# Performance work log

Measured on AMD Instinct MI355X. Metric: run time of the kernel, lower is better.

Reference implementation:

```python
import jax, jax.numpy as jnp
import numpy as np

N, E = 100000, 1600000
IN_C, OUT_C, H, EDGE_DIM = 128, 64, 2, 4
NEG_SLOPE = 0.2
LN_EPS = 1e-5


def setup_inputs() -> dict:
    key = jax.random.key(0)
    ks = jax.random.split(key, 12)
    s = 1.0 / np.sqrt(IN_C)
    inp = {
        "x": jax.random.normal(ks[0], (N, IN_C), jnp.float32),
        "edge_index": jax.random.randint(ks[1], (2, E), 0, N, jnp.int64),
        "edge_attr": jax.random.normal(ks[2], (E, EDGE_DIM), jnp.float32),
        "W": jax.random.normal(ks[3], (IN_C, H * OUT_C), jnp.float32) * s,
        "att_src": jax.random.normal(ks[4], (H, OUT_C), jnp.float32) * s,
        "att_dst": jax.random.normal(ks[5], (H, OUT_C), jnp.float32) * s,
        "W_edge": jax.random.normal(ks[6], (EDGE_DIM, H * OUT_C), jnp.float32) * 0.5,
        "att_edge": jax.random.normal(ks[7], (H, OUT_C), jnp.float32) * s,
        "bias": jnp.zeros((OUT_C,), jnp.float32),
        "gamma": jnp.ones((OUT_C,), jnp.float32),
        "beta": jnp.zeros((OUT_C,), jnp.float32),
    }
    return inp


def reference(x, edge_index, edge_attr, W, att_src, att_dst, W_edge, att_edge, bias, gamma, beta):
    n = x.shape[0]
    src, dst = edge_index[0], edge_index[1]
    # shared src/dst linear (PyG GATConv with single input tensor)
    h = (x @ W).reshape(n, H, OUT_C)                       # [N,H,C]
    a_src = jnp.einsum("nhc,hc->nh", h, att_src)          # [N,H]
    a_dst = jnp.einsum("nhc,hc->nh", h, att_dst)          # [N,H]
    e = (edge_attr @ W_edge).reshape(-1, H, OUT_C)         # [E,H,C]
    a_edge = jnp.einsum("ehc,hc->eh", e, att_edge)        # [E,H]
    alpha = jax.nn.leaky_relu(a_src[src] + a_dst[dst] + a_edge, NEG_SLOPE)  # [E,H]
    # segment softmax over edges grouped by destination node
    amax = jax.ops.segment_max(alpha, dst, num_segments=n)
    ex = jnp.exp(alpha - amax[dst])
    denom = jax.ops.segment_sum(ex, dst, num_segments=n)
    w = ex / (denom[dst] + 1e-16)                          # [E,H]
    msg = h[src] * w[:, :, None]                           # [E,H,C]
    out = jax.ops.segment_sum(msg, dst, num_segments=n)    # [N,H,C]
    out = out.mean(axis=1) + bias                          # concat=False -> head mean
    # LayerNorm + ReLU
    mu = out.mean(-1, keepdims=True)
    var = ((out - mu) ** 2).mean(-1, keepdims=True)
    out = (out - mu) * jax.lax.rsqrt(var + LN_EPS) * gamma + beta
    return jax.nn.relu(out)
```

## Files before the change

### kernel.cpp

```cpp
#include <hip/hip_runtime.h>
#include <hip/hip_fp16.h>
#include <math.h>

#define IN_C 128
#define HC   128
#define OUT_C 64
#define NEG_SLOPE 0.2f
#define LN_EPS 1e-5f
#define CHUNK 4096
#define BSH   8
#define BMSK  255
#define NBMAX 512
#define NB2MAX 1024

typedef __attribute__((ext_vector_type(8))) short bf16x8;
typedef __attribute__((ext_vector_type(4))) float f32x4;

__device__ inline unsigned bf16pack(float a, float b) {
    unsigned ua = __float_as_uint(a), ub = __float_as_uint(b);
    ua = (ua + 0x7fffu + ((ua >> 16) & 1u)) >> 16;
    ub = (ub + 0x7fffu + ((ub >> 16) & 1u)) >> 16;
    return ua | (ub << 16);
}

__global__ __launch_bounds__(256) void k_pre(const float* __restrict__ W,
                                             const float* __restrict__ W_edge,
                                             const float* __restrict__ att_edge,
                                             const int* __restrict__ ei_dst,
                                             unsigned short* __restrict__ WbfT,
                                             float* __restrict__ V,
                                             int* __restrict__ off,
                                             int E, int NB, int PB) {
    __shared__ int hist[NBMAX];
    int b = blockIdx.x, t = threadIdx.x;
    if (b < 8) {
        #pragma unroll
        for (int i = 0; i < 8; ++i) {
            int idx = b * 2048 + i * 256 + t;
            int k = idx >> 7, col = idx & 127;
            unsigned u = __float_as_uint(W[idx]);
            WbfT[col * 128 + k] =
                (unsigned short)((u + 0x7fffu + ((u >> 16) & 1u)) >> 16);
        }
        return;
    }
    if (b == 8) {
        if (t < 8) {
            int d = t >> 1, h = t & 1;
            float s = 0.f;
            for (int c = 0; c < 64; ++c)
                s += W_edge[d * HC + h * 64 + c] * att_edge[h * 64 + c];
            V[d * 2 + h] = s;
        }
        return;
    }
    int pb = b - 9;
    for (int i = t; i < NB; i += 256) hist[i] = 0;
    __syncthreads();
    int base = pb * CHUNK;
    int lim = E - base; if (lim > CHUNK) lim = CHUNK;
    if (lim == CHUNK) {
        #pragma unroll
        for (int u = 0; u < 4; ++u) {
            int4 v = *(const int4*)&ei_dst[base + u * 1024 + t * 4];
            atomicAdd(&hist[v.x >> BSH], 1);
            atomicAdd(&hist[v.y >> BSH], 1);
            atomicAdd(&hist[v.z >> BSH], 1);
            atomicAdd(&hist[v.w >> BSH], 1);
        }
    } else {
        for (int i = t; i < lim; i += 256)
            atomicAdd(&hist[ei_dst[base + i] >> BSH], 1);
    }
    __syncthreads();
    for (int i = t; i < NB; i += 256)
        off[(size_t)i * PB + pb] = hist[i];
}

__global__ __launch_bounds__(256) void k_scan(int* __restrict__ off,
                                              int* __restrict__ bsum, int nS) {
    __shared__ int sm[256];
    int t = threadIdx.x;
    int base = blockIdx.x * 1024 + t * 4;
    int v0 = 0, v1 = 0, v2 = 0, v3 = 0;
    if (base + 0 < nS) v0 = off[base + 0];
    if (base + 1 < nS) v1 = off[base + 1];
    if (base + 2 < nS) v2 = off[base + 2];
    if (base + 3 < nS) v3 = off[base + 3];
    int s = v0 + v1 + v2 + v3;
    sm[t] = s;
    __syncthreads();
    for (int o = 1; o < 256; o <<= 1) {
        int u = (t >= o) ? sm[t - o] : 0;
        __syncthreads();
        sm[t] += u;
        __syncthreads();
    }
    int excl = sm[t] - s;
    if (base + 0 < nS) off[base + 0] = excl;
    if (base + 1 < nS) off[base + 1] = excl + v0;
    if (base + 2 < nS) off[base + 2] = excl + v0 + v1;
    if (base + 3 < nS) off[base + 3] = excl + v0 + v1 + v2;
    if (t == 255) bsum[blockIdx.x] = sm[255];
}

__device__ inline void scan_bsum(const int* __restrict__ bsum, int nb2,
                                 int* bs, int* sm, int t) {
    int v0 = (4 * t + 0 < nb2) ? bsum[4 * t + 0] : 0;
    int v1 = (4 * t + 1 < nb2) ? bsum[4 * t + 1] : 0;
    int v2 = (4 * t + 2 < nb2) ? bsum[4 * t + 2] : 0;
    int v3 = (4 * t + 3 < nb2) ? bsum[4 * t + 3] : 0;
    int s = v0 + v1 + v2 + v3;
    sm[t] = s;
    __syncthreads();
    for (int o = 1; o < 256; o <<= 1) {
        int u = (t >= o) ? sm[t - o] : 0;
        __syncthreads();
        sm[t] += u;
        __syncthreads();
    }
    int excl = sm[t] - s;
    bs[4 * t + 0] = excl;
    bs[4 * t + 1] = excl + v0;
    bs[4 * t + 2] = excl + v0 + v1;
    bs[4 * t + 3] = excl + v0 + v1 + v2;
    __syncthreads();
}

__global__ __launch_bounds__(256) void k_fused(
        const float* __restrict__ x,
        const unsigned short* __restrict__ WbfT,
        const float* __restrict__ attS, const float* __restrict__ attD,
        unsigned* __restrict__ hb,
        float* __restrict__ a_src, float* __restrict__ a_dst, int M,
        const int* __restrict__ ei, const float* __restrict__ ea,
        const float* __restrict__ V,
        const int* __restrict__ off, const int* __restrict__ bsum,
        int* __restrict__ bsum2, uint2* __restrict__ pA,
        int E, int NB, int PB, int nb2, int GB) {
    __shared__ unsigned xb[64 * 64];
    const int t = threadIdx.x;
    const int bid = blockIdx.x;
    const int r5 = bid % 5, g5 = bid / 5;

    if (r5 == 4) {
        int* cur = (int*)xb;
        int* bs  = (int*)xb + NBMAX;
        int* sm  = (int*)xb + NBMAX + NB2MAX;
        int pb = g5;
        scan_bsum(bsum, nb2, bs, sm, t);
        if (pb == 0)
            for (int i = t; i < nb2; i += 256) bsum2[i] = bs[i];
        for (int i = t; i < NB; i += 256) {
            size_t oi = (size_t)i * PB + pb;
            cur[i] = off[oi] + bs[(int)(oi >> 10)];
        }
        __syncthreads();
        float v0 = V[0], v1 = V[1], v2 = V[2], v3 = V[3];
        float v4 = V[4], v5 = V[5], v6 = V[6], v7 = V[7];
        int base = pb * CHUNK;
        int lim = E - base; if (lim > CHUNK) lim = CHUNK;
        if (lim == CHUNK) {
            #pragma unroll
            for (int h = 0; h < 2; ++h) {
                int e0 = base + h * 2048 + t;
                int sA[8], dA[8];
                #pragma unroll
                for (int k = 0; k < 8; ++k) {
                    sA[k] = ei[e0 + k * 256];
                    dA[k] = ei[E + e0 + k * 256];
                }
                float4 aA[8];
                #pragma unroll
                for (int k = 0; k < 8; ++k)
                    aA[k] = ((const float4*)ea)[e0 + k * 256];
                #pragma unroll
                for (int k = 0; k < 8; ++k) {
                    float ae0 = aA[k].x * v0 + aA[k].y * v2 + aA[k].z * v4 + aA[k].w * v6;
                    float ae1 = aA[k].x * v1 + aA[k].y * v3 + aA[k].z * v5 + aA[k].w * v7;
                    __half2 hx = __floats2half2_rn(ae0, ae1);
                    int slot = atomicAdd(&cur[dA[k] >> BSH], 1);
                    pA[slot] = make_uint2(
                        (unsigned)sA[k] | ((unsigned)(dA[k] & BMSK) << 17),
                        *reinterpret_cast<unsigned*>(&hx));
                }
            }
        } else {
            for (int i = t; i < lim; i += 256) {
                int e = base + i;
                int s = ei[e], d = ei[E + e];
                float4 a = ((const float4*)ea)[e];
                float ae0 = a.x * v0 + a.y * v2 + a.z * v4 + a.w * v6;
                float ae1 = a.x * v1 + a.y * v3 + a.z * v5 + a.w * v7;
                __half2 hx = __floats2half2_rn(ae0, ae1);
                int slot = atomicAdd(&cur[d >> BSH], 1);
                pA[slot] = make_uint2((unsigned)s | ((unsigned)(d & BMSK) << 17),
                                      *reinterpret_cast<unsigned*>(&hx));
            }
        }
        return;
    }

    const int gid = g5 * 4 + r5;
    if (gid >= GB) return;
    const int brow = gid * 64;
    const float4* x4 = (const float4*)x;
    #pragma unroll
    for (int i = 0; i < 8; ++i) {
        int idx = i * 256 + t;
        int row = idx >> 5, c4 = idx & 31;
        float4 v = make_float4(0.f, 0.f, 0.f, 0.f);
        if (brow + row < M) v = x4[(size_t)(brow + row) * 32 + c4];
        unsigned lo = bf16pack(v.x, v.y), hi = bf16pack(v.z, v.w);
        int byte = row * 256 + ((c4 * 8) ^ ((row & 7) << 4));
        *(uint2*)((char*)xb + byte) = make_uint2(lo, hi);
    }
    __syncthreads();

    const int w = t >> 6, lane = t & 63;
    const int col = lane & 15, qr = lane >> 4;
    f32x4 acc[8];
    #pragma unroll
    for (int ct = 0; ct < 8; ++ct) acc[ct] = (f32x4){0.f, 0.f, 0.f, 0.f};

    const int arow = w * 16 + col;
    #pragma unroll
    for (int ks = 0; ks < 4; ++ks) {
        int abyte = arow * 256 + ((ks * 64 + qr * 16) ^ ((arow & 7) << 4));
        bf16x8 af = *(const bf16x8*)((const char*)xb + abyte);
        #pragma unroll
        for (int ct = 0; ct < 8; ++ct) {
            bf16x8 bfr = *(const bf16x8*)&WbfT[(size_t)(ct * 16 + col) * 128 + ks * 32 + qr * 8];
            acc[ct] = __builtin_amdgcn_mfma_f32_16x16x32_bf16(af, bfr, acc[ct], 0, 0, 0);
        }
    }

    float pS0[4], pS1[4], pD0[4], pD1[4];
    #pragma unroll
    for (int r = 0; r < 4; ++r) { pS0[r] = pS1[r] = pD0[r] = pD1[r] = 0.f; }
    #pragma unroll
    for (int ct = 0; ct < 8; ++ct) {
        float s = attS[ct * 16 + col], d = attD[ct * 16 + col];
        #pragma unroll
        for (int r = 0; r < 4; ++r) {
            float a = acc[ct][r];
            if (ct < 4) { pS0[r] += a * s; pD0[r] += a * d; }
            else        { pS1[r] += a * s; pD1[r] += a * d; }
        }
    }
    #pragma unroll
    for (int m = 1; m < 16; m <<= 1) {
        #pragma unroll
        for (int r = 0; r < 4; ++r) {
            pS0[r] += __shfl_xor(pS0[r], m);
            pS1[r] += __shfl_xor(pS1[r], m);
            pD0[r] += __shfl_xor(pD0[r], m);
            pD1[r] += __shfl_xor(pD1[r], m);
        }
    }
    #pragma unroll
    for (int r = 0; r < 4; ++r) {
        int grow = brow + w * 16 + qr * 4 + r;
        if (grow < M) {
            if (col == 0) {
                a_src[2 * grow + 0] = pS0[r];
                a_src[2 * grow + 1] = pS1[r];
                a_dst[2 * grow + 0] = pD0[r];
                a_dst[2 * grow + 1] = pD1[r];
            }
            #pragma unroll
            for (int ct = 0; ct < 4; ++ct)
                hb[(size_t)grow * 64 + ct * 16 + col] =
                    bf16pack(acc[ct][r], acc[ct + 4][r]);
        }
    }
}

__global__ __launch_bounds__(256) void k_csr(const uint2* __restrict__ pA,
                                             const int* __restrict__ off,
                                             const int* __restrict__ bsum2,
                                             const float* __restrict__ a_src,
                                             const float* __restrict__ a_dst,
                                             int* __restrict__ rowptr,
                                             uint2* __restrict__ payload,
                                             int M, int E, int NB, int PB) {
    __shared__ int cnt[256];
    __shared__ int sc[256];
    __shared__ int cur[256];
    __shared__ float2 adl[256];
    int b = blockIdx.x, t = threadIdx.x;
    int n0 = b << BSH;
    int nloc = M - n0; if (nloc > 256) nloc = 256;

    size_t o0 = (size_t)b * PB;
    int s0 = off[o0] + bsum2[(int)(o0 >> 10)];
    int s1 = E;
    if (b + 1 < NB) {
        size_t o1 = (size_t)(b + 1) * PB;
        s1 = off[o1] + bsum2[(int)(o1 >> 10)];
    }
    cnt[t] = 0;
    if (t < nloc) adl[t] = ((const float2*)a_dst)[n0 + t];
    __syncthreads();

    for (int i = s0 + t; i < s1; i += 256)
        atomicAdd(&cnt[(pA[i].x >> 17) & BMSK], 1);
    __syncthreads();
    int c = cnt[t];
    sc[t] = c;
    __syncthreads();
    for (int o = 1; o < 256; o <<= 1) {
        int u = (t >= o) ? sc[t - o] : 0;
        __syncthreads();
        sc[t] += u;
        __syncthreads();
    }
    {
        int base = s0 + sc[t] - c;
        cur[t] = base;
        if (t < nloc) rowptr[n0 + t] = base;
    }
    if (b == NB - 1 && t == 0) rowptr[M] = E;
    __syncthreads();
    for (int i = s0 + t; i < s1; i += 256) {
        uint2 p = pA[i];
        int src = p.x & 0x1FFFF;
        int dl = (p.x >> 17) & BMSK;
        __half2 aeh = *reinterpret_cast<__half2*>(&p.y);
        float2 as = ((const float2*)a_src)[src];
        float2 ad = adl[dl];
        float al0 = as.x + ad.x + __low2float(aeh);
        al0 = al0 > 0.f ? al0 : NEG_SLOPE * al0;
        float al1 = as.y + ad.y + __high2float(aeh);
        al1 = al1 > 0.f ? al1 : NEG_SLOPE * al1;
        __half2 hx = __floats2half2_rn(__expf(al0), __expf(al1));
        int pos = atomicAdd(&cur[dl], 1);
        payload[pos] = make_uint2((unsigned)src, *reinterpret_cast<unsigned*>(&hx));
    }
}

__global__ __launch_bounds__(256) void k_gather(const uint2* __restrict__ payload,
                                                const int* __restrict__ rowptr,
                                                const unsigned* __restrict__ hb,
                                                const float* __restrict__ bias,
                                                const float* __restrict__ gamma,
                                                const float* __restrict__ beta,
                                                float* __restrict__ out, int M) {
    __shared__ uint2 stg[4][64];
    int w = threadIdx.x >> 6, lane = threadIdx.x & 63;
    int n = blockIdx.x * 4 + w;
    if (n >= M) return;
    int beg = rowptr[n], end = rowptr[n + 1];
    float acc0 = 0.f, acc1 = 0.f, pe0 = 0.f, pe1 = 0.f;

    for (int base = beg; base < end; base += 64) {
        int cnt = end - base; if (cnt > 64) cnt = 64;
        uint2 p = make_uint2(0u, 0u);
        if (lane < cnt) p = payload[base + lane];
        stg[w][lane] = p;
        {
            __half2 he = *reinterpret_cast<__half2*>(&p.y);
            pe0 += __low2float(he);
            pe1 += __high2float(he);
        }
        int j = 0;
        for (; j + 8 <= cnt; j += 8) {
            uint2 q0 = stg[w][j + 0], q1 = stg[w][j + 1];
            uint2 q2 = stg[w][j + 2], q3 = stg[w][j + 3];
            uint2 q4 = stg[w][j + 4], q5 = stg[w][j + 5];
            uint2 q6 = stg[w][j + 6], q7 = stg[w][j + 7];
            int s0 = __builtin_amdgcn_readfirstlane((int)q0.x);
            int s1 = __builtin_amdgcn_readfirstlane((int)q1.x);
            int s2 = __builtin_amdgcn_readfirstlane((int)q2.x);
            int s3 = __builtin_amdgcn_readfirstlane((int)q3.x);
            int s4 = __builtin_amdgcn_readfirstlane((int)q4.x);
            int s5 = __builtin_amdgcn_readfirstlane((int)q5.x);
            int s6 = __builtin_amdgcn_readfirstlane((int)q6.x);
            int s7 = __builtin_amdgcn_readfirstlane((int)q7.x);
            unsigned h0 = (hb + (size_t)s0 * 64)[lane];
            unsigned h1 = (hb + (size_t)s1 * 64)[lane];
            unsigned h2 = (hb + (size_t)s2 * 64)[lane];
            unsigned h3 = (hb + (size_t)s3 * 64)[lane];
            unsigned h4 = (hb + (size_t)s4 * 64)[lane];
            unsigned h5 = (hb + (size_t)s5 * 64)[lane];
            unsigned h6 = (hb + (size_t)s6 * 64)[lane];
            unsigned h7 = (hb + (size_t)s7 * 64)[lane];
            __half2 e0 = *reinterpret_cast<__half2*>(&q0.y);
            __half2 e1 = *reinterpret_cast<__half2*>(&q1.y);
            __half2 e2 = *reinterpret_cast<__half2*>(&q2.y);
            __half2 e3 = *reinterpret_cast<__half2*>(&q3.y);
            __half2 e4 = *reinterpret_cast<__half2*>(&q4.y);
            __half2 e5 = *reinterpret_cast<__half2*>(&q5.y);
            __half2 e6 = *reinterpret_cast<__half2*>(&q6.y);
            __half2 e7 = *reinterpret_cast<__half2*>(&q7.y);
            acc0 += __low2float(e0)  * __uint_as_float(h0 << 16);
            acc1 += __high2float(e0) * __uint_as_float(h0 & 0xffff0000u);
            acc0 += __low2float(e1)  * __uint_as_float(h1 << 16);
            acc1 += __high2float(e1) * __uint_as_float(h1 & 0xffff0000u);
            acc0 += __low2float(e2)  * __uint_as_float(h2 << 16);
            acc1 += __high2float(e2) * __uint_as_float(h2 & 0xffff0000u);
            acc0 += __low2float(e3)  * __uint_as_float(h3 << 16);
            acc1 += __high2float(e3) * __uint_as_float(h3 & 0xffff0000u);
            acc0 += __low2float(e4)  * __uint_as_float(h4 << 16);
            acc1 += __high2float(e4) * __uint_as_float(h4 & 0xffff0000u);
            acc0 += __low2float(e5)  * __uint_as_float(h5 << 16);
            acc1 += __high2float(e5) * __uint_as_float(h5 & 0xffff0000u);
            acc0 += __low2float(e6)  * __uint_as_float(h6 << 16);
            acc1 += __high2float(e6) * __uint_as_float(h6 & 0xffff0000u);
            acc0 += __low2float(e7)  * __uint_as_float(h7 << 16);
            acc1 += __high2float(e7) * __uint_as_float(h7 & 0xffff0000u);
        }
        for (; j + 4 <= cnt; j += 4) {
            uint2 q0 = stg[w][j + 0], q1 = stg[w][j + 1];
            uint2 q2 = stg[w][j + 2], q3 = stg[w][j + 3];
            int s0 = __builtin_amdgcn_readfirstlane((int)q0.x);
            int s1 = __builtin_amdgcn_readfirstlane((int)q1.x);
            int s2 = __builtin_amdgcn_readfirstlane((int)q2.x);
            int s3 = __builtin_amdgcn_readfirstlane((int)q3.x);
            unsigned h0 = (hb + (size_t)s0 * 64)[lane];
            unsigned h1 = (hb + (size_t)s1 * 64)[lane];
            unsigned h2 = (hb + (size_t)s2 * 64)[lane];
            unsigned h3 = (hb + (size_t)s3 * 64)[lane];
            __half2 e0 = *reinterpret_cast<__half2*>(&q0.y);
            __half2 e1 = *reinterpret_cast<__half2*>(&q1.y);
            __half2 e2 = *reinterpret_cast<__half2*>(&q2.y);
            __half2 e3 = *reinterpret_cast<__half2*>(&q3.y);
            acc0 += __low2float(e0)  * __uint_as_float(h0 << 16);
            acc1 += __high2float(e0) * __uint_as_float(h0 & 0xffff0000u);
            acc0 += __low2float(e1)  * __uint_as_float(h1 << 16);
            acc1 += __high2float(e1) * __uint_as_float(h1 & 0xffff0000u);
            acc0 += __low2float(e2)  * __uint_as_float(h2 << 16);
            acc1 += __high2float(e2) * __uint_as_float(h2 & 0xffff0000u);
            acc0 += __low2float(e3)  * __uint_as_float(h3 << 16);
            acc1 += __high2float(e3) * __uint_as_float(h3 & 0xffff0000u);
        }
        for (; j < cnt; ++j) {
            uint2 q0 = stg[w][j];
            int s0 = __builtin_amdgcn_readfirstlane((int)q0.x);
            unsigned h0 = (hb + (size_t)s0 * 64)[lane];
            __half2 e0 = *reinterpret_cast<__half2*>(&q0.y);
            acc0 += __low2float(e0)  * __uint_as_float(h0 << 16);
            acc1 += __high2float(e0) * __uint_as_float(h0 & 0xffff0000u);
        }
    }

    float d0 = pe0, d1 = pe1;
    #pragma unroll
    for (int m = 32; m; m >>= 1) {
        d0 += __shfl_xor(d0, m);
        d1 += __shfl_xor(d1, m);
    }

    float o = 0.5f * (acc0 / (d0 + 1e-16f) + acc1 / (d1 + 1e-16f)) + bias[lane];
    float mu = o;
    #pragma unroll
    for (int m = 32; m; m >>= 1) mu += __shfl_xor(mu, m);
    mu *= (1.f / 64.f);
    float c = o - mu;
    float v = c * c;
    #pragma unroll
    for (int m = 32; m; m >>= 1) v += __shfl_xor(v, m);
    v *= (1.f / 64.f);
    float y = c * rsqrtf(v + LN_EPS) * gamma[lane] + beta[lane];
    out[(size_t)n * OUT_C + lane] = fmaxf(y, 0.f);
}

extern "C" void kernel_launch(void* const* d_in, const int* in_sizes, int n_in,
                              void* d_out, int out_size, void* d_ws, size_t ws_size,
                              hipStream_t stream) {
    const float* x     = (const float*)d_in[0];
    const int*   ei    = (const int*)d_in[1];
    const float* ea    = (const float*)d_in[2];
    const float* W     = (const float*)d_in[3];
    const float* attS  = (const float*)d_in[4];
    const float* attD  = (const float*)d_in[5];
    const float* We    = (const float*)d_in[6];
    const float* attE  = (const float*)d_in[7];
    const float* bias  = (const float*)d_in[8];
    const float* gamma = (const float*)d_in[9];
    const float* beta  = (const float*)d_in[10];

    const int M  = in_sizes[0] / IN_C;
    const int E  = in_sizes[1] / 2;
    const int NB = (M + BMSK) >> BSH;
    const int PB = (E + CHUNK - 1) / CHUNK;
    const int nS = NB * PB;
    const int nb2 = (nS + 1023) / 1024;
    const int GB = (M + 63) / 64;

    char* ws = (char*)d_ws;
    size_t woff = 0;
    auto alloc = [&](size_t bytes) -> void* {
        void* p = ws + woff;
        woff += (bytes + 255) & ~(size_t)255;
        return p;
    };
    unsigned*       hb     = (unsigned*)      alloc((size_t)M * 64 * 4);
    float*          a_src  = (float*)         alloc((size_t)M * 2 * 4);
    float*          a_dst  = (float*)         alloc((size_t)M * 2 * 4);
    int*            off    = (int*)           alloc((size_t)nS * 4);
    int*            bsum   = (int*)           alloc((size_t)nb2 * 4);
    int*            bsum2  = (int*)           alloc((size_t)nb2 * 4);
    int*            rowptr = (int*)           alloc((size_t)(M + 1) * 4);
    uint2*          pA     = (uint2*)         alloc((size_t)E * 8);
    uint2*          payload= (uint2*)         alloc((size_t)E * 8);
    unsigned short* WbfT   = (unsigned short*)alloc(128 * 128 * 2);
    float*          V      = (float*)         alloc(32);

    k_pre<<<9 + PB, 256, 0, stream>>>(W, We, attE, ei + E, WbfT, V, off, E, NB, PB);
    k_scan<<<nb2, 256, 0, stream>>>(off, bsum, nS);
    k_fused<<<5 * PB, 256, 0, stream>>>(x, WbfT, attS, attD, hb, a_src, a_dst, M,
                                        ei, ea, V, off, bsum, bsum2, pA,
                                        E, NB, PB, nb2, GB);
    k_csr<<<NB, 256, 0, stream>>>(pA, off, bsum2, a_src, a_dst, rowptr, payload,
                                  M, E, NB, PB);
    k_gather<<<(M + 3) / 4, 256, 0, stream>>>(payload, rowptr, hb, bias, gamma, beta,
                                              (float*)d_out, M);
}
```

Baseline: 144.1 us.

## Split fused partition/GEMM kernel into separate launches with persistent double-buffered GEMM

The single interleaved kernel, which ran edge partitioning and the node-feature GEMM in alternating blocks, becomes two kernels. The partitioning now runs alone, followed by a persistent GEMM kernel with a fixed grid of 391 blocks. Each GEMM block walks tiles with a stride and prefetches the next x tile into registers while computing the current one, using a double-buffered shared-memory tile. This gives up the overlap between partitioning and GEMM that the fused launch provided, adds one more kernel launch, and hides x load latency behind MFMA work inside the GEMM.

```diff
diff --git a/kernel.cpp b/kernel.cpp
--- a/kernel.cpp
+++ b/kernel.cpp
@@ -12,6 +12,7 @@
 #define BMSK  255
 #define NBMAX 512
 #define NB2MAX 1024
+#define NGB   391
 
 typedef __attribute__((ext_vector_type(8))) short bf16x8;
 typedef __attribute__((ext_vector_type(4))) float f32x4;
@@ -127,152 +128,187 @@
     __syncthreads();
 }
 
-__global__ __launch_bounds__(256) void k_fused(
-        const float* __restrict__ x,
-        const unsigned short* __restrict__ WbfT,
-        const float* __restrict__ attS, const float* __restrict__ attD,
-        unsigned* __restrict__ hb,
-        float* __restrict__ a_src, float* __restrict__ a_dst, int M,
-        const int* __restrict__ ei, const float* __restrict__ ea,
-        const float* __restrict__ V,
-        const int* __restrict__ off, const int* __restrict__ bsum,
-        int* __restrict__ bsum2, uint2* __restrict__ pA,
-        int E, int NB, int PB, int nb2, int GB) {
-    __shared__ unsigned xb[64 * 64];
+__global__ __launch_bounds__(256) void k_part(const int* __restrict__ ei,
+                                              const float* __restrict__ ea,
+                                              const float* __restrict__ V,
+                                              const int* __restrict__ off,
+                                              const int* __restrict__ bsum,
+                                              int* __restrict__ bsum2,
+                                              uint2* __restrict__ pA,
+                                              int E, int NB, int PB, int nb2) {
+    __shared__ int cur[NBMAX];
+    __shared__ int bs[NB2MAX];
+    __shared__ int sm[256];
+    int pb = blockIdx.x, t = threadIdx.x;
+
+    scan_bsum(bsum, nb2, bs, sm, t);
+    if (pb == 0)
+        for (int i = t; i < nb2; i += 256) bsum2[i] = bs[i];
+
+    for (int i = t; i < NB; i += 256) {
+        size_t oi = (size_t)i * PB + pb;
+        cur[i] = off[oi] + bs[(int)(oi >> 10)];
+    }
+    __syncthreads();
+    float v0 = V[0], v1 = V[1], v2 = V[2], v3 = V[3];
+    float v4 = V[4], v5 = V[5], v6 = V[6], v7 = V[7];
+    int base = pb * CHUNK;
+    int lim = E - base; if (lim > CHUNK) lim = CHUNK;
+    if (lim == CHUNK) {
+        #pragma unroll
+        for (int h = 0; h < 2; ++h) {
+            int e0 = base + h * 2048 + t;
+            int sA[8], dA[8];
+            #pragma unroll
+            for (int k = 0; k < 8; ++k) {
+                sA[k] = ei[e0 + k * 256];
+                dA[k] = ei[E + e0 + k * 256];
+            }
+            float4 aA[8];
+            #pragma unroll
+            for (int k = 0; k < 8; ++k)
+                aA[k] = ((const float4*)ea)[e0 + k * 256];
+            #pragma unroll
+            for (int k = 0; k < 8; ++k) {
+                float ae0 = aA[k].x * v0 + aA[k].y * v2 + aA[k].z * v4 + aA[k].w * v6;
+                float ae1 = aA[k].x * v1 + aA[k].y * v3 + aA[k].z * v5 + aA[k].w * v7;
+                __half2 hx = __floats2half2_rn(ae0, ae1);
+                int slot = atomicAdd(&cur[dA[k] >> BSH], 1);
+                pA[slot] = make_uint2(
+                    (unsigned)sA[k] | ((unsigned)(dA[k] & BMSK) << 17),
+                    *reinterpret_cast<unsigned*>(&hx));
+            }
+        }
+    } else {
+        for (int i = t; i < lim; i += 256) {
+            int e = base + i;
+            int s = ei[e], d = ei[E + e];
+            float4 a = ((const float4*)ea)[e];
+            float ae0 = a.x * v0 + a.y * v2 + a.z * v4 + a.w * v6;
+            float ae1 = a.x * v1 + a.y * v3 + a.z * v5 + a.w * v7;
+            __half2 hx = __floats2half2_rn(ae0, ae1);
+            int slot = atomicAdd(&cur[d >> BSH], 1);
+            pA[slot] = make_uint2((unsigned)s | ((unsigned)(d & BMSK) << 17),
+                                  *reinterpret_cast<unsigned*>(&hx));
+        }
+    }
+}
+
+__global__ __launch_bounds__(256) void k_gemm(const float* __restrict__ x,
+                                              const unsigned short* __restrict__ WbfT,
+                                              const float* __restrict__ attS,
+                                              const float* __restrict__ attD,
+                                              unsigned* __restrict__ hb,
+                                              float* __restrict__ a_src,
+                                              float* __restrict__ a_dst,
+                                              int M, int T, int stride) {
+    __shared__ unsigned xb[2][64 * 64];
     const int t = threadIdx.x;
-    const int bid = blockIdx.x;
-    const int r5 = bid % 5, g5 = bid / 5;
-
-    if (r5 == 4) {
-        int* cur = (int*)xb;
-        int* bs  = (int*)xb + NBMAX;
-        int* sm  = (int*)xb + NBMAX + NB2MAX;
-        int pb = g5;
-        scan_bsum(bsum, nb2, bs, sm, t);
-        if (pb == 0)
-            for (int i = t; i < nb2; i += 256) bsum2[i] = bs[i];
-        for (int i = t; i < NB; i += 256) {
-            size_t oi = (size_t)i * PB + pb;
-            cur[i] = off[oi] + bs[(int)(oi >> 10)];
-        }
-        __syncthreads();
-        float v0 = V[0], v1 = V[1], v2 = V[2], v3 = V[3];
-        float v4 = V[4], v5 = V[5], v6 = V[6], v7 = V[7];
-        int base = pb * CHUNK;
-        int lim = E - base; if (lim > CHUNK) lim = CHUNK;
-        if (lim == CHUNK) {
-            #pragma unroll
-            for (int h = 0; h < 2; ++h) {
-                int e0 = base + h * 2048 + t;
-                int sA[8], dA[8];
-                #pragma unroll
-                for (int k = 0; k < 8; ++k) {
-                    sA[k] = ei[e0 + k * 256];
-                    dA[k] = ei[E + e0 + k * 256];
-                }
-                float4 aA[8];
-                #pragma unroll
-                for (int k = 0; k < 8; ++k)
-                    aA[k] = ((const float4*)ea)[e0 + k * 256];
-                #pragma unroll
-                for (int k = 0; k < 8; ++k) {
-                    float ae0 = aA[k].x * v0 + aA[k].y * v2 + aA[k].z * v4 + aA[k].w * v6;
-                    float ae1 = aA[k].x * v1 + aA[k].y * v3 + aA[k].z * v5 + aA[k].w * v7;
-                    __half2 hx = __floats2half2_rn(ae0, ae1);
-                    int slot = atomicAdd(&cur[dA[k] >> BSH], 1);
-                    pA[slot] = make_uint2(
-                        (unsigned)sA[k] | ((unsigned)(dA[k] & BMSK) << 17),
-                        *reinterpret_cast<unsigned*>(&hx));
-                }
-            }
-        } else {
-            for (int i = t; i < lim; i += 256) {
-                int e = base + i;
-                int s = ei[e], d = ei[E + e];
-                float4 a = ((const float4*)ea)[e];
-                float ae0 = a.x * v0 + a.y * v2 + a.z * v4 + a.w * v6;
-                float ae1 = a.x * v1 + a.y * v3 + a.z * v5 + a.w * v7;
-                __half2 hx = __floats2half2_rn(ae0, ae1);
-                int slot = atomicAdd(&cur[d >> BSH], 1);
-                pA[slot] = make_uint2((unsigned)s | ((unsigned)(d & BMSK) << 17),
-                                      *reinterpret_cast<unsigned*>(&hx));
-            }
-        }
-        return;
-    }
-
-    const int gid = g5 * 4 + r5;
-    if (gid >= GB) return;
-    const int brow = gid * 64;
     const float4* x4 = (const float4*)x;
-    #pragma unroll
-    for (int i = 0; i < 8; ++i) {
-        int idx = i * 256 + t;
-        int row = idx >> 5, c4 = idx & 31;
-        float4 v = make_float4(0.f, 0.f, 0.f, 0.f);
-        if (brow + row < M) v = x4[(size_t)(brow + row) * 32 + c4];
-        unsigned lo = bf16pack(v.x, v.y), hi = bf16pack(v.z, v.w);
-        int byte = row * 256 + ((c4 * 8) ^ ((row & 7) << 4));
-        *(uint2*)((char*)xb + byte) = make_uint2(lo, hi);
-    }
-    __syncthreads();
-
     const int w = t >> 6, lane = t & 63;
     const int col = lane & 15, qr = lane >> 4;
-    f32x4 acc[8];
-    #pragma unroll
-    for (int ct = 0; ct < 8; ++ct) acc[ct] = (f32x4){0.f, 0.f, 0.f, 0.f};
-
-    const int arow = w * 16 + col;
-    #pragma unroll
-    for (int ks = 0; ks < 4; ++ks) {
-        int abyte = arow * 256 + ((ks * 64 + qr * 16) ^ ((arow & 7) << 4));
-        bf16x8 af = *(const bf16x8*)((const char*)xb + abyte);
-        #pragma unroll
-        for (int ct = 0; ct < 8; ++ct) {
-            bf16x8 bfr = *(const bf16x8*)&WbfT[(size_t)(ct * 16 + col) * 128 + ks * 32 + qr * 8];
-            acc[ct] = __builtin_amdgcn_mfma_f32_16x16x32_bf16(af, bfr, acc[ct], 0, 0, 0);
-        }
-    }
-
-    float pS0[4], pS1[4], pD0[4], pD1[4];
-    #pragma unroll
-    for (int r = 0; r < 4; ++r) { pS0[r] = pS1[r] = pD0[r] = pD1[r] = 0.f; }
+    const int srow = t >> 5, sc4 = t & 31;
+
+    float sv[8], dv[8];
     #pragma unroll
     for (int ct = 0; ct < 8; ++ct) {
-        float s = attS[ct * 16 + col], d = attD[ct * 16 + col];
+        sv[ct] = attS[ct * 16 + col];
+        dv[ct] = attD[ct * 16 + col];
+    }
+
+    auto LOAD = [&](int tile, float4* lr) {
+        int brow = tile * 64;
+        #pragma unroll
+        for (int i = 0; i < 8; ++i) {
+            int row = brow + srow + i * 8;
+            lr[i] = (row < M) ? x4[(size_t)row * 32 + sc4]
+                              : make_float4(0.f, 0.f, 0.f, 0.f);
+        }
+    };
+    auto STORE = [&](int buf, const float4* lr) {
+        #pragma unroll
+        for (int i = 0; i < 8; ++i) {
+            int row = srow + i * 8;
+            unsigned lo = bf16pack(lr[i].x, lr[i].y);
+            unsigned hi = bf16pack(lr[i].z, lr[i].w);
+            int byte = row * 256 + ((sc4 * 8) ^ ((row & 7) << 4));
+            *(uint2*)((char*)xb[buf] + byte) = make_uint2(lo, hi);
+        }
+    };
+    auto COMPUTE = [&](int buf, int tile) {
+        const int brow = tile * 64;
+        f32x4 acc[8];
+        #pragma unroll
+        for (int ct = 0; ct < 8; ++ct) acc[ct] = (f32x4){0.f, 0.f, 0.f, 0.f};
+        const int arow = w * 16 + col;
+        #pragma unroll
+        for (int ks = 0; ks < 4; ++ks) {
+            int abyte = arow * 256 + ((ks * 64 + qr * 16) ^ ((arow & 7) << 4));
+            bf16x8 af = *(const bf16x8*)((const char*)xb[buf] + abyte);
+            #pragma unroll
+            for (int ct = 0; ct < 8; ++ct) {
+                bf16x8 bfr = *(const bf16x8*)&WbfT[(size_t)(ct * 16 + col) * 128 + ks * 32 + qr * 8];
+                acc[ct] = __builtin_amdgcn_mfma_f32_16x16x32_bf16(af, bfr, acc[ct], 0, 0, 0);
+            }
+        }
+        float pS0[4], pS1[4], pD0[4], pD1[4];
+        #pragma unroll
+        for (int r = 0; r < 4; ++r) { pS0[r] = pS1[r] = pD0[r] = pD1[r] = 0.f; }
+        #pragma unroll
+        for (int ct = 0; ct < 8; ++ct) {
+            #pragma unroll
+            for (int r = 0; r < 4; ++r) {
+                float a = acc[ct][r];
+                if (ct < 4) { pS0[r] += a * sv[ct]; pD0[r] += a * dv[ct]; }
+                else        { pS1[r] += a * sv[ct]; pD1[r] += a * dv[ct]; }
+            }
+        }
+        #pragma unroll
+        for (int m = 1; m < 16; m <<= 1) {
+            #pragma unroll
+            for (int r = 0; r < 4; ++r) {
+                pS0[r] += __shfl_xor(pS0[r], m);
+                pS1[r] += __shfl_xor(pS1[r], m);
+                pD0[r] += __shfl_xor(pD0[r], m);
+                pD1[r] += __shfl_xor(pD1[r], m);
+            }
+        }
         #pragma unroll
         for (int r = 0; r < 4; ++r) {
-            float a = acc[ct][r];
-            if (ct < 4) { pS0[r] += a * s; pD0[r] += a * d; }
-            else        { pS1[r] += a * s; pD1[r] += a * d; }
-        }
-    }
-    #pragma unroll
-    for (int m = 1; m < 16; m <<= 1) {
-        #pragma unroll
-        for (int r = 0; r < 4; ++r) {
-            pS0[r] += __shfl_xor(pS0[r], m);
-            pS1[r] += __shfl_xor(pS1[r], m);
-            pD0[r] += __shfl_xor(pD0[r], m);
-            pD1[r] += __shfl_xor(pD1[r], m);
-        }
-    }
-    #pragma unroll
-    for (int r = 0; r < 4; ++r) {
-        int grow = brow + w * 16 + qr * 4 + r;
-        if (grow < M) {
-            if (col == 0) {
-                a_src[2 * grow + 0] = pS0[r];
-                a_src[2 * grow + 1] = pS1[r];
-                a_dst[2 * grow + 0] = pD0[r];
-                a_dst[2 * grow + 1] = pD1[r];
+            int grow = brow + w * 16 + qr * 4 + r;
+            if (grow < M) {
+                if (col == 0) {
+                    a_src[2 * grow + 0] = pS0[r];
+                    a_src[2 * grow + 1] = pS1[r];
+                    a_dst[2 * grow + 0] = pD0[r];
+                    a_dst[2 * grow + 1] = pD1[r];
+                }
+                #pragma unroll
+                for (int ct = 0; ct < 4; ++ct)
+                    hb[(size_t)grow * 64 + ct * 16 + col] =
+                        bf16pack(acc[ct][r], acc[ct + 4][r]);
             }
-            #pragma unroll
-            for (int ct = 0; ct < 4; ++ct)
-                hb[(size_t)grow * 64 + ct * 16 + col] =
-                    bf16pack(acc[ct][r], acc[ct + 4][r]);
-        }
+        }
+    };
+
+    int tile = blockIdx.x;
+    if (tile >= T) return;
+    float4 lr[8];
+    LOAD(tile, lr);
+    STORE(0, lr);
+    __syncthreads();
+    int cur = 0;
+    for (;;) {
+        int nxt = tile + stride;
+        float4 nr[8];
+        bool hasN = (nxt < T);
+        if (hasN) LOAD(nxt, nr);
+        COMPUTE(cur, tile);
+        if (!hasN) break;
+        STORE(cur ^ 1, nr);
+        __syncthreads();
+        cur ^= 1;
+        tile = nxt;
     }
 }
 
@@ -486,7 +522,7 @@
     const int PB = (E + CHUNK - 1) / CHUNK;
     const int nS = NB * PB;
     const int nb2 = (nS + 1023) / 1024;
-    const int GB = (M + 63) / 64;
+    const int T  = (M + 63) / 64;
 
     char* ws = (char*)d_ws;
     size_t woff = 0;
@@ -509,9 +545,8 @@
 
     k_pre<<<9 + PB, 256, 0, stream>>>(W, We, attE, ei + E, WbfT, V, off, E, NB, PB);
     k_scan<<<nb2, 256, 0, stream>>>(off, bsum, nS);
-    k_fused<<<5 * PB, 256, 0, stream>>>(x, WbfT, attS, attD, hb, a_src, a_dst, M,
-                                        ei, ea, V, off, bsum, bsum2, pA,
-                                        E, NB, PB, nb2, GB);
+    k_part<<<PB, 256, 0, stream>>>(ei, ea, V, off, bsum, bsum2, pA, E, NB, PB, nb2);
+    k_gemm<<<NGB, 256, 0, stream>>>(x, WbfT, attS, attD, hb, a_src, a_dst, M, T, NGB);
     k_csr<<<NB, 256, 0, stream>>>(pA, off, bsum2, a_src, a_dst, rowptr, payload,
                                   M, E, NB, PB);
     k_gather<<<(M + 3) / 4, 256, 0, stream>>>(payload, rowptr, hb, bias, gamma, beta,
```

New measurement: 154.9 us. 7.5% more time.
